# Optimization experiments

Measured on AMD Instinct MI355X. Metric: run time of the kernel, lower is better.

## Reference

```python
import jax, jax.numpy as jnp
import numpy as np

N_NODES = 100000
N_EDGES = 1600000
IN_FEATS = 128
H_FEATS = 128


def setup_inputs() -> dict:
    key = jax.random.key(0)
    ks = jax.random.split(key, 8)
    in_feat = jax.random.normal(ks[0], (N_NODES, IN_FEATS), dtype=jnp.float32)
    src = jax.random.randint(ks[1], (N_EDGES,), 0, N_NODES, dtype=jnp.int32)
    dst = jax.random.randint(ks[2], (N_EDGES,), 0, N_NODES, dtype=jnp.int32)
    # GraphConv weights are (in, out); xavier-ish scaling
    W1 = jax.random.normal(ks[3], (IN_FEATS, 2 * H_FEATS), dtype=jnp.float32) * (2.0 / (IN_FEATS + 2 * H_FEATS)) ** 0.5
    b1 = jnp.zeros((2 * H_FEATS,), dtype=jnp.float32)
    W2 = jax.random.normal(ks[4], (2 * H_FEATS, H_FEATS), dtype=jnp.float32) * (2.0 / (3 * H_FEATS)) ** 0.5
    b2 = jnp.zeros((H_FEATS,), dtype=jnp.float32)
    fc1_w = jax.random.normal(ks[5], (H_FEATS, H_FEATS), dtype=jnp.float32) * (1.0 / H_FEATS) ** 0.5
    fc2_w = jax.random.normal(ks[6], (H_FEATS, H_FEATS), dtype=jnp.float32) * (1.0 / H_FEATS) ** 0.5
    return {"in_feat": in_feat, "src": src, "dst": dst, "W1": W1, "b1": b1,
            "W2": W2, "b2": b2, "fc1_w": fc1_w, "fc2_w": fc2_w}


def _degrees(src, dst):
    ones = jnp.ones((src.shape[0],), dtype=jnp.float32)
    out_deg = jax.ops.segment_sum(ones, src, num_segments=N_NODES)
    in_deg = jax.ops.segment_sum(ones, dst, num_segments=N_NODES)
    # DGL norm='both': clamp degree to >= 1
    return jnp.clip(out_deg, 1.0), jnp.clip(in_deg, 1.0)


def _graph_conv(x, W, b, src, dst, out_norm, in_norm):
    # norm='both': scale src feats by D_out^{-1/2}, sum-aggregate, scale by D_in^{-1/2}
    # DGL applies W first when in_feats > out_feats (saves memory/flops)
    if W.shape[0] > W.shape[1]:
        x = x @ W
        x = x * out_norm[:, None]
        agg = jax.ops.segment_sum(x[src], dst, num_segments=N_NODES)
        rst = agg * in_norm[:, None]
    else:
        x = x * out_norm[:, None]
        agg = jax.ops.segment_sum(x[src], dst, num_segments=N_NODES)
        rst = (agg * in_norm[:, None]) @ W
    return rst + b


def reference(in_feat, src, dst, W1, b1, W2, b2, fc1_w, fc2_w):
    out_deg, in_deg = _degrees(src, dst)
    out_norm = jax.lax.rsqrt(out_deg)
    in_norm = jax.lax.rsqrt(in_deg)
    h = _graph_conv(in_feat, W1, b1, src, dst, out_norm, in_norm)
    h = jax.nn.relu(h)
    h = _graph_conv(h, W2, b2, src, dst, out_norm, in_norm)
    h = jax.nn.relu(h)
    feat1 = h @ fc1_w.T  # nn.Linear, bias=False
    feat2 = h @ fc2_w.T
    return (h, feat1, feat2)
```

## Files before the change

### kernel.cpp

```cpp
#include <hip/hip_runtime.h>

#define N_NODES 100000
#define N_EDGES 1600000
#define P_PARTS 8
#define S_SLICES 128
#define NP 12500
#define ES 12500
#define FEAT2_OFF 12800000

typedef __attribute__((ext_vector_type(8))) short short8;
typedef __attribute__((ext_vector_type(8))) unsigned short ushort8v;
typedef __attribute__((ext_vector_type(4))) float f32x4;

__device__ inline float bf2f(unsigned short h) {
    union { unsigned int u; float f; } v; v.u = ((unsigned int)h) << 16; return v.f;
}
__device__ inline unsigned short f2bf(float f) {
    union { unsigned int u; float f; } v; v.f = f;
    unsigned int u = v.u;
    return (unsigned short)((u + 0x7fffu + ((u >> 16) & 1u)) >> 16);
}

__global__ __launch_bounds__(256) void hist_part_kernel(
    const int* __restrict__ src, const int* __restrict__ dst,
    int* __restrict__ part_src, int* __restrict__ part_dst) {
    __shared__ int h[NP];
    int tid = threadIdx.x;
    int p = blockIdx.x & (P_PARTS - 1), s = blockIdx.x >> 3;
    for (int j = tid; j < NP; j += 256) h[j] = 0;
    __syncthreads();
    int lo = p * NP;
    const int4* s4 = (const int4*)(src + s * ES);
    const int4* d4 = (const int4*)(dst + s * ES);
    for (int i = tid; i < ES / 4; i += 256) {
        int4 sv = s4[i];
        int4 dv = d4[i];
        int a;
        a = sv.x - lo; if ((unsigned)a < NP) atomicAdd(&h[a], 1);
        a = sv.y - lo; if ((unsigned)a < NP) atomicAdd(&h[a], 1);
        a = sv.z - lo; if ((unsigned)a < NP) atomicAdd(&h[a], 1);
        a = sv.w - lo; if ((unsigned)a < NP) atomicAdd(&h[a], 1);
        a = dv.x - lo; if ((unsigned)a < NP) atomicAdd(&h[a], 0x10000);
        a = dv.y - lo; if ((unsigned)a < NP) atomicAdd(&h[a], 0x10000);
        a = dv.z - lo; if ((unsigned)a < NP) atomicAdd(&h[a], 0x10000);
        a = dv.w - lo; if ((unsigned)a < NP) atomicAdd(&h[a], 0x10000);
    }
    __syncthreads();
    int* ps = part_src + (size_t)(p * S_SLICES + s) * NP;
    int* pd = part_dst + (size_t)(p * S_SLICES + s) * NP;
    for (int j = tid; j < NP; j += 256) {
        unsigned v = (unsigned)h[j];
        ps[j] = (int)(v & 0xFFFFu);
        pd[j] = (int)(v >> 16);
    }
}

__global__ void reduce_prefix_norm_kernel(const int* __restrict__ part_src,
                                          int* __restrict__ part_dst,
                                          int* __restrict__ deg_in,
                                          float* __restrict__ out_norm,
                                          float* __restrict__ in_norm) {
    int n = blockIdx.x * blockDim.x + threadIdx.x;
    if (n >= N_NODES) return;
    int p = n / NP, j = n - p * NP;
    size_t base = (size_t)p * S_SLICES * NP + j;
    int so = 0;
    for (int s = 0; s < S_SLICES; s++) so += part_src[base + (size_t)s * NP];
    int run = 0;
    for (int s = 0; s < S_SLICES; s++) {
        int c = part_dst[base + (size_t)s * NP];
        part_dst[base + (size_t)s * NP] = run;
        run += c;
    }
    deg_in[n] = run;
    out_norm[n] = rsqrtf((float)(so < 1 ? 1 : so));
    in_norm[n]  = rsqrtf((float)(run < 1 ? 1 : run));
}

__global__ void scan_kernel(const int* __restrict__ deg, int* __restrict__ row_ptr) {
    __shared__ int sums[1024];
    int t = threadIdx.x;
    int s = 0;
    if (t < 1000) {
        const int4* d4 = (const int4*)(deg + t * 100);
        #pragma unroll
        for (int i = 0; i < 25; i++) { int4 v = d4[i]; s += v.x + v.y + v.z + v.w; }
    }
    sums[t] = s;
    __syncthreads();
    for (int st = 1; st < 1024; st <<= 1) {
        int v = (t >= st) ? sums[t - st] : 0;
        __syncthreads();
        sums[t] += v;
        __syncthreads();
    }
    if (t < 1000) {
        int base = (t == 0) ? 0 : sums[t - 1];
        for (int i = 0; i < 100; i++) { row_ptr[t * 100 + i] = base; base += deg[t * 100 + i]; }
    }
    if (t == 1023) row_ptr[N_NODES] = sums[1023];
}

__global__ __launch_bounds__(256) void fill_part_kernel(
    const int* __restrict__ src, const int* __restrict__ dst,
    const int* __restrict__ row_ptr, const int* __restrict__ part_dst,
    int* __restrict__ csr_src) {
    __shared__ int cnt[NP / 2];
    int tid = threadIdx.x;
    int p = blockIdx.x & (P_PARTS - 1), s = blockIdx.x >> 3;
    for (int j = tid; j < NP / 2; j += 256) cnt[j] = 0;
    __syncthreads();
    int lo = p * NP;
    const int* pd = part_dst + (size_t)(p * S_SLICES + s) * NP;
    const int4* s4 = (const int4*)(src + s * ES);
    const int4* d4 = (const int4*)(dst + s * ES);
    for (int i = tid; i < ES / 4; i += 256) {
        int4 sv = s4[i];
        int4 dv = d4[i];
        int a;
        a = dv.x - lo;
        if ((unsigned)a < NP) {
            int sh = (a & 1) << 4;
            int old = atomicAdd(&cnt[a >> 1], 1 << sh);
            int r = (old >> sh) & 0xFFFF;
            csr_src[row_ptr[lo + a] + pd[a] + r] = sv.x;
        }
        a = dv.y - lo;
        if ((unsigned)a < NP) {
            int sh = (a & 1) << 4;
            int old = atomicAdd(&cnt[a >> 1], 1 << sh);
            int r = (old >> sh) & 0xFFFF;
            csr_src[row_ptr[lo + a] + pd[a] + r] = sv.y;
        }
        a = dv.z - lo;
        if ((unsigned)a < NP) {
            int sh = (a & 1) << 4;
            int old = atomicAdd(&cnt[a >> 1], 1 << sh);
            int r = (old >> sh) & 0xFFFF;
            csr_src[row_ptr[lo + a] + pd[a] + r] = sv.z;
        }
        a = dv.w - lo;
        if ((unsigned)a < NP) {
            int sh = (a & 1) << 4;
            int old = atomicAdd(&cnt[a >> 1], 1 << sh);
            int r = (old >> sh) & 0xFFFF;
            csr_src[row_ptr[lo + a] + pd[a] + r] = sv.w;
        }
    }
}

__global__ void prep_weights_kernel(const float* __restrict__ W1, const float* __restrict__ W2,
                                    const float* __restrict__ fc1, const float* __restrict__ fc2,
                                    unsigned short* __restrict__ Wt1, unsigned short* __restrict__ Wt2,
                                    unsigned short* __restrict__ fcb) {
    int idx = blockIdx.x * blockDim.x + threadIdx.x;
    if (idx < 32768) {
        int n = idx >> 7, k = idx & 127;
        Wt1[idx] = f2bf(W1[k * 256 + n]);
    } else if (idx < 65536) {
        int t = idx - 32768;
        int n = t >> 8, k = t & 255;
        Wt2[t] = f2bf(W2[k * 128 + n]);
    } else if (idx < 98304) {
        int t = idx - 65536;
        fcb[t] = f2bf(t < 16384 ? fc1[t] : fc2[t - 16384]);
    }
}

__global__ void prescale_kernel(const float4* __restrict__ in, const float* __restrict__ out_norm,
                                ushort4* __restrict__ out) {
    int idx = blockIdx.x * blockDim.x + threadIdx.x;
    if (idx >= N_NODES * 32) return;
    float sc = out_norm[idx >> 5];
    float4 v = in[idx];
    ushort4 o;
    o.x = f2bf(v.x * sc); o.y = f2bf(v.y * sc); o.z = f2bf(v.z * sc); o.w = f2bf(v.w * sc);
    out[idx] = o;
}

template<int EPI>
__global__ __launch_bounds__(256) void aggregate_bf(
    const unsigned short* __restrict__ x, const int* __restrict__ row_ptr,
    const int* __restrict__ csr_src, const float* __restrict__ in_norm,
    const float* __restrict__ b2, float4* __restrict__ outF,
    unsigned short* __restrict__ outB) {
    int wave = threadIdx.x >> 6, lane = threadIdx.x & 63;
    int n = blockIdx.x * 4 + wave;
    if (n >= N_NODES) return;
    int q = lane >> 4, ql = lane & 15;
    int s0 = row_ptr[n], s1 = row_ptr[n + 1];
    const ushort8v* xf = (const ushort8v*)x;
    float a0[8], a1[8];
    #pragma unroll
    for (int j = 0; j < 8; j++) { a0[j] = 0.f; a1[j] = 0.f; }
    int i = s0 + q;
    for (; i + 12 < s1; i += 16) {
        int sA = csr_src[i],     sB = csr_src[i + 4];
        int sC = csr_src[i + 8], sD = csr_src[i + 12];
        ushort8v va = xf[(size_t)sA * 16 + ql];
        ushort8v vb = xf[(size_t)sB * 16 + ql];
        ushort8v vc = xf[(size_t)sC * 16 + ql];
        ushort8v vd = xf[(size_t)sD * 16 + ql];
        #pragma unroll
        for (int j = 0; j < 8; j++) a0[j] += bf2f(va[j]) + bf2f(vc[j]);
        #pragma unroll
        for (int j = 0; j < 8; j++) a1[j] += bf2f(vb[j]) + bf2f(vd[j]);
    }
    for (; i < s1; i += 4) {
        ushort8v va = xf[(size_t)csr_src[i] * 16 + ql];
        #pragma unroll
        for (int j = 0; j < 8; j++) a0[j] += bf2f(va[j]);
    }
    #pragma unroll
    for (int j = 0; j < 8; j++) {
        float v = a0[j] + a1[j];
        v += __shfl_xor(v, 16);
        v += __shfl_xor(v, 32);
        a0[j] = v;
    }
    float inn = in_norm[n];
    if (EPI == 0) {
        if (q == 0) {
            ushort8v o;
            #pragma unroll
            for (int j = 0; j < 8; j++) o[j] = f2bf(a0[j] * inn);
            ((ushort8v*)outB)[(size_t)n * 16 + ql] = o;
        }
    } else {
        const float4* b4 = (const float4*)b2;
        float4 blo = b4[ql * 2], bhi = b4[ql * 2 + 1];
        float v[8];
        v[0] = fmaxf(fmaf(a0[0], inn, blo.x), 0.f);
        v[1] = fmaxf(fmaf(a0[1], inn, blo.y), 0.f);
        v[2] = fmaxf(fmaf(a0[2], inn, blo.z), 0.f);
        v[3] = fmaxf(fmaf(a0[3], inn, blo.w), 0.f);
        v[4] = fmaxf(fmaf(a0[4], inn, bhi.x), 0.f);
        v[5] = fmaxf(fmaf(a0[5], inn, bhi.y), 0.f);
        v[6] = fmaxf(fmaf(a0[6], inn, bhi.z), 0.f);
        v[7] = fmaxf(fmaf(a0[7], inn, bhi.w), 0.f);
        if (q == 0) {
            ushort8v o;
            #pragma unroll
            for (int j = 0; j < 8; j++) o[j] = f2bf(v[j]);
            ((ushort8v*)outB)[(size_t)n * 16 + ql] = o;
        } else if (q == 1) {
            outF[(size_t)n * 32 + ql * 2] = make_float4(v[0], v[1], v[2], v[3]);
        } else if (q == 2) {
            outF[(size_t)n * 32 + ql * 2 + 1] = make_float4(v[4], v[5], v[6], v[7]);
        }
    }
}

template<int K, int NF, int EPI>
__global__ __launch_bounds__(256) void gemm_mfma(
    const unsigned short* __restrict__ A, const unsigned short* __restrict__ Bt,
    const float* __restrict__ aux, void* __restrict__ Cv, int ldc, int M) {
    constexpr int CH = K / 8;
    __shared__ short blds[NF * 16 * K];
    int tid = threadIdx.x;
    int bn = blockIdx.x * (NF * 16);
    int bm = blockIdx.y * 128;
    {
        const short8* g = (const short8*)Bt;
        short8* l = (short8*)blds;
        for (int id = tid; id < NF * 16 * CH; id += 256) {
            int col = id / CH, kc = id % CH;
            l[col * CH + (kc ^ (col & (CH - 1)))] = g[(size_t)(bn + col) * CH + kc];
        }
    }
    __syncthreads();
    int wm = tid >> 6, lane = tid & 63;
    int lr = lane & 15, kq = lane >> 4;
    int r0 = bm + wm * 32 + lr;
    int r1 = r0 + 16;
    const short8* A8 = (const short8*)A;
    size_t a0row = (size_t)(r0 < M ? r0 : 0) * CH;
    size_t a1row = (size_t)(r1 < M ? r1 : 0) * CH;
    const short8* l8 = (const short8*)blds;

    f32x4 acc[2][NF];
    #pragma unroll
    for (int m = 0; m < 2; m++)
        #pragma unroll
        for (int j = 0; j < NF; j++) acc[m][j] = (f32x4)0.f;

    short8 a0 = A8[a0row + kq];
    short8 a1 = A8[a1row + kq];
    for (int kc2 = 0; kc2 < K / 32; kc2++) {
        int kc = kc2 * 4 + kq;
        short8 n0, n1;
        if (kc2 + 1 < K / 32) {
            n0 = A8[a0row + kc + 4];
            n1 = A8[a1row + kc + 4];
        }
        #pragma unroll
        for (int nj = 0; nj < NF; nj++) {
            int col = nj * 16 + lr;
            short8 b = l8[col * CH + (kc ^ (col & (CH - 1)))];
            acc[0][nj] = __builtin_amdgcn_mfma_f32_16x16x32_bf16(a0, b, acc[0][nj], 0, 0, 0);
            acc[1][nj] = __builtin_amdgcn_mfma_f32_16x16x32_bf16(a1, b, acc[1][nj], 0, 0, 0);
        }
        a0 = n0; a1 = n1;
    }

    #pragma unroll
    for (int mi = 0; mi < 2; mi++) {
        #pragma unroll
        for (int i = 0; i < 4; i++) {
            int gr = bm + wm * 32 + mi * 16 + kq * 4 + i;
            if (gr >= M) continue;
            float sc = (EPI == 2) ? aux[gr] : 0.f;
            #pragma unroll
            for (int nj = 0; nj < NF; nj++) {
                int col = bn + nj * 16 + lr;
                float v = acc[mi][nj][i];
                if (EPI == 1)
                    ((unsigned short*)Cv)[(size_t)gr * ldc + col] = f2bf(fmaxf(v + aux[col], 0.f));
                else if (EPI == 2)
                    ((unsigned short*)Cv)[(size_t)gr * ldc + col] = f2bf(v * sc);
                else {
                    float* dstp = (float*)Cv + (size_t)(col >= 128 ? FEAT2_OFF : 0)
                                  + (size_t)gr * 128 + (col & 127);
                    *dstp = v;
                }
            }
        }
    }
}

extern "C" void kernel_launch(void* const* d_in, const int* in_sizes, int n_in,
                              void* d_out, int out_size, void* d_ws, size_t ws_size,
                              hipStream_t stream) {
    const float* in_feat = (const float*)d_in[0];
    const int*   src     = (const int*)d_in[1];
    const int*   dst     = (const int*)d_in[2];
    const float* W1      = (const float*)d_in[3];
    const float* b1      = (const float*)d_in[4];
    const float* W2      = (const float*)d_in[5];
    const float* b2      = (const float*)d_in[6];
    const float* fc1_w   = (const float*)d_in[7];
    const float* fc2_w   = (const float*)d_in[8];

    float* out = (float*)d_out;
    float* h_out = out;
    float* feat1 = out + (size_t)12800000;
    unsigned short* xs_bf   = (unsigned short*)out;
    unsigned short* agg1_bf = (unsigned short*)(out + 6400000);
    unsigned short* h1_bf   = (unsigned short*)(out + 12800000);
    unsigned short* x2_bf   = (unsigned short*)(out + 25600000);

    int* part_dst = (int*)d_ws;
    int* part_src = part_dst + P_PARTS * S_SLICES * NP;
    int* csr_src  = part_src;
    int* deg_in   = part_src + P_PARTS * S_SLICES * NP;
    int* row_ptr  = deg_in + 100000;
    float* out_norm = (float*)(row_ptr + 100004);
    float* in_norm  = out_norm + 100000;
    unsigned short* Wt1 = (unsigned short*)(in_norm + 100000);
    unsigned short* Wt2 = Wt1 + 32768;
    unsigned short* fcb = Wt2 + 32768;
    unsigned short* h_bf = fcb + 32768;

    hist_part_kernel<<<P_PARTS * S_SLICES, 256, 0, stream>>>(src, dst, part_src, part_dst);
    reduce_prefix_norm_kernel<<<(N_NODES + 255) / 256, 256, 0, stream>>>(
        part_src, part_dst, deg_in, out_norm, in_norm);
    scan_kernel<<<1, 1024, 0, stream>>>(deg_in, row_ptr);
    fill_part_kernel<<<P_PARTS * S_SLICES, 256, 0, stream>>>(src, dst, row_ptr, part_dst, csr_src);

    prep_weights_kernel<<<384, 256, 0, stream>>>(W1, W2, fc1_w, fc2_w, Wt1, Wt2, fcb);

    prescale_kernel<<<12500, 256, 0, stream>>>((const float4*)in_feat, out_norm, (ushort4*)xs_bf);

    aggregate_bf<0><<<25000, 256, 0, stream>>>(xs_bf, row_ptr, csr_src,
                                               in_norm, nullptr, nullptr, agg1_bf);

    gemm_mfma<128, 16, 1><<<dim3(1, 782), 256, 0, stream>>>(agg1_bf, Wt1, b1, h1_bf, 256, N_NODES);
    gemm_mfma<256, 8, 2><<<dim3(1, 782), 256, 0, stream>>>(h1_bf, Wt2, out_norm, x2_bf, 128, N_NODES);

    aggregate_bf<1><<<25000, 256, 0, stream>>>(x2_bf, row_ptr, csr_src,
                                               in_norm, b2, (float4*)h_out, h_bf);

    gemm_mfma<128, 16, 3><<<dim3(1, 782), 256, 0, stream>>>(h_bf, fcb, nullptr, feat1, 128, N_NODES);
}
```

Measured before the change: 399.0 us.

## Shrink partition histograms to u16, unroll aggregate tail, double GEMM block rows

The per-partition degree histograms and their prefix offsets are now stored as 16-bit values instead of 32-bit, which halves the traffic of the hist, reduce and fill passes. The aggregation tail loop is unrolled by two into separate accumulators to expose more memory parallelism. The GEMM kernels now launch 512 threads per block covering 256 rows, so each LDS-staged weight tile is reused across twice as many rows. The u16 storage assumes per-slice counts and per-node in-degree prefixes stay below 65536, and the larger blocks halve the block count, which may reduce occupancy.

```diff
diff --git a/kernel.cpp b/kernel.cpp
--- a/kernel.cpp
+++ b/kernel.cpp
@@ -23,7 +23,7 @@
 
 __global__ __launch_bounds__(256) void hist_part_kernel(
     const int* __restrict__ src, const int* __restrict__ dst,
-    int* __restrict__ part_src, int* __restrict__ part_dst) {
+    unsigned short* __restrict__ part_src, unsigned short* __restrict__ part_dst) {
     __shared__ int h[NP];
     int tid = threadIdx.x;
     int p = blockIdx.x & (P_PARTS - 1), s = blockIdx.x >> 3;
@@ -46,17 +46,17 @@
         a = dv.w - lo; if ((unsigned)a < NP) atomicAdd(&h[a], 0x10000);
     }
     __syncthreads();
-    int* ps = part_src + (size_t)(p * S_SLICES + s) * NP;
-    int* pd = part_dst + (size_t)(p * S_SLICES + s) * NP;
+    unsigned short* ps = part_src + (size_t)(p * S_SLICES + s) * NP;
+    unsigned short* pd = part_dst + (size_t)(p * S_SLICES + s) * NP;
     for (int j = tid; j < NP; j += 256) {
         unsigned v = (unsigned)h[j];
-        ps[j] = (int)(v & 0xFFFFu);
-        pd[j] = (int)(v >> 16);
-    }
-}
-
-__global__ void reduce_prefix_norm_kernel(const int* __restrict__ part_src,
-                                          int* __restrict__ part_dst,
+        ps[j] = (unsigned short)(v & 0xFFFFu);
+        pd[j] = (unsigned short)(v >> 16);
+    }
+}
+
+__global__ void reduce_prefix_norm_kernel(const unsigned short* __restrict__ part_src,
+                                          unsigned short* __restrict__ part_dst,
                                           int* __restrict__ deg_in,
                                           float* __restrict__ out_norm,
                                           float* __restrict__ in_norm) {
@@ -69,7 +69,7 @@
     int run = 0;
     for (int s = 0; s < S_SLICES; s++) {
         int c = part_dst[base + (size_t)s * NP];
-        part_dst[base + (size_t)s * NP] = run;
+        part_dst[base + (size_t)s * NP] = (unsigned short)run;
         run += c;
     }
     deg_in[n] = run;
@@ -103,7 +103,7 @@
 
 __global__ __launch_bounds__(256) void fill_part_kernel(
     const int* __restrict__ src, const int* __restrict__ dst,
-    const int* __restrict__ row_ptr, const int* __restrict__ part_dst,
+    const int* __restrict__ row_ptr, const unsigned short* __restrict__ part_dst,
     int* __restrict__ csr_src) {
     __shared__ int cnt[NP / 2];
     int tid = threadIdx.x;
@@ -111,7 +111,7 @@
     for (int j = tid; j < NP / 2; j += 256) cnt[j] = 0;
     __syncthreads();
     int lo = p * NP;
-    const int* pd = part_dst + (size_t)(p * S_SLICES + s) * NP;
+    const unsigned short* pd = part_dst + (size_t)(p * S_SLICES + s) * NP;
     const int4* s4 = (const int4*)(src + s * ES);
     const int4* d4 = (const int4*)(dst + s * ES);
     for (int i = tid; i < ES / 4; i += 256) {
@@ -206,7 +206,16 @@
         #pragma unroll
         for (int j = 0; j < 8; j++) a1[j] += bf2f(vb[j]) + bf2f(vd[j]);
     }
-    for (; i < s1; i += 4) {
+    for (; i + 4 < s1; i += 8) {
+        int sA = csr_src[i], sB = csr_src[i + 4];
+        ushort8v va = xf[(size_t)sA * 16 + ql];
+        ushort8v vb = xf[(size_t)sB * 16 + ql];
+        #pragma unroll
+        for (int j = 0; j < 8; j++) a0[j] += bf2f(va[j]);
+        #pragma unroll
+        for (int j = 0; j < 8; j++) a1[j] += bf2f(vb[j]);
+    }
+    if (i < s1) {
         ushort8v va = xf[(size_t)csr_src[i] * 16 + ql];
         #pragma unroll
         for (int j = 0; j < 8; j++) a0[j] += bf2f(va[j]);
@@ -252,18 +261,18 @@
 }
 
 template<int K, int NF, int EPI>
-__global__ __launch_bounds__(256) void gemm_mfma(
+__global__ __launch_bounds__(512) void gemm_mfma(
     const unsigned short* __restrict__ A, const unsigned short* __restrict__ Bt,
     const float* __restrict__ aux, void* __restrict__ Cv, int ldc, int M) {
     constexpr int CH = K / 8;
     __shared__ short blds[NF * 16 * K];
     int tid = threadIdx.x;
     int bn = blockIdx.x * (NF * 16);
-    int bm = blockIdx.y * 128;
+    int bm = blockIdx.y * 256;
     {
         const short8* g = (const short8*)Bt;
         short8* l = (short8*)blds;
-        for (int id = tid; id < NF * 16 * CH; id += 256) {
+        for (int id = tid; id < NF * 16 * CH; id += 512) {
             int col = id / CH, kc = id % CH;
             l[col * CH + (kc ^ (col & (CH - 1)))] = g[(size_t)(bn + col) * CH + kc];
         }
@@ -349,10 +358,10 @@
     unsigned short* h1_bf   = (unsigned short*)(out + 12800000);
     unsigned short* x2_bf   = (unsigned short*)(out + 25600000);
 
-    int* part_dst = (int*)d_ws;
-    int* part_src = part_dst + P_PARTS * S_SLICES * NP;
-    int* csr_src  = part_src;
-    int* deg_in   = part_src + P_PARTS * S_SLICES * NP;
+    unsigned short* part_dst = (unsigned short*)d_ws;
+    unsigned short* part_src = part_dst + (size_t)P_PARTS * S_SLICES * NP;
+    int* csr_src  = (int*)part_src;
+    int* deg_in   = (int*)(part_src + (size_t)P_PARTS * S_SLICES * NP);
     int* row_ptr  = deg_in + 100000;
     float* out_norm = (float*)(row_ptr + 100004);
     float* in_norm  = out_norm + 100000;
@@ -374,11 +383,11 @@
     aggregate_bf<0><<<25000, 256, 0, stream>>>(xs_bf, row_ptr, csr_src,
                                                in_norm, nullptr, nullptr, agg1_bf);
 
-    gemm_mfma<128, 16, 1><<<dim3(1, 782), 256, 0, stream>>>(agg1_bf, Wt1, b1, h1_bf, 256, N_NODES);
-    gemm_mfma<256, 8, 2><<<dim3(1, 782), 256, 0, stream>>>(h1_bf, Wt2, out_norm, x2_bf, 128, N_NODES);
+    gemm_mfma<128, 16, 1><<<dim3(1, 391), 512, 0, stream>>>(agg1_bf, Wt1, b1, h1_bf, 256, N_NODES);
+    gemm_mfma<256, 8, 2><<<dim3(1, 391), 512, 0, stream>>>(h1_bf, Wt2, out_norm, x2_bf, 128, N_NODES);
 
     aggregate_bf<1><<<25000, 256, 0, stream>>>(x2_bf, row_ptr, csr_src,
                                                in_norm, b2, (float4*)h_out, h_bf);
 
-    gemm_mfma<128, 16, 3><<<dim3(1, 782), 256, 0, stream>>>(h_bf, fcb, nullptr, feat1, 128, N_NODES);
-}
+    gemm_mfma<128, 16, 3><<<dim3(1, 391), 512, 0, stream>>>(h_bf, fcb, nullptr, feat1, 128, N_NODES);
+}
```

New measurement: 346.5 us (median of 3 runs). 13.2% less time.
